# Performance work log

Hardware: AMD Instinct MI355X
Metric: run time of the kernel (lower is better)

Reference implementation:

```python
import jax, jax.numpy as jnp
import numpy as np

B, L, D, W = 4, 512, 768, 12
K = L * W  # number of candidate spans


def _mlp(x, w1, b1, w2, b2):
    # Linear -> ReLU -> (Dropout=identity in eval) -> Linear
    return jax.nn.relu(x @ w1.T + b1) @ w2.T + b2


def setup_inputs() -> dict:
    key = jax.random.key(0)
    ks = jax.random.split(key, 16)
    sc_d = 1.0 / np.sqrt(D)
    sc_4d = 1.0 / np.sqrt(4 * D)
    sc_2d = 1.0 / np.sqrt(2 * D)
    inp = {
        "h": jax.random.normal(ks[0], (B, L, D), dtype=jnp.float32),
        "span_idx": jax.random.randint(ks[1], (B, K, 2), 0, L, dtype=jnp.int64),
        # project_start: Linear(D,4D), Linear(4D,D)
        "ws1": jax.random.uniform(ks[2], (4 * D, D), jnp.float32, -sc_d, sc_d),
        "bs1": jax.random.uniform(ks[3], (4 * D,), jnp.float32, -sc_d, sc_d),
        "ws2": jax.random.uniform(ks[4], (D, 4 * D), jnp.float32, -sc_4d, sc_4d),
        "bs2": jax.random.uniform(ks[5], (D,), jnp.float32, -sc_4d, sc_4d),
        # project_end
        "we1": jax.random.uniform(ks[6], (4 * D, D), jnp.float32, -sc_d, sc_d),
        "be1": jax.random.uniform(ks[7], (4 * D,), jnp.float32, -sc_d, sc_d),
        "we2": jax.random.uniform(ks[8], (D, 4 * D), jnp.float32, -sc_4d, sc_4d),
        "be2": jax.random.uniform(ks[9], (D,), jnp.float32, -sc_4d, sc_4d),
        # out_project: Linear(2D,4D), Linear(4D,D)
        "wo1": jax.random.uniform(ks[10], (4 * D, 2 * D), jnp.float32, -sc_2d, sc_2d),
        "bo1": jax.random.uniform(ks[11], (4 * D,), jnp.float32, -sc_2d, sc_2d),
        "wo2": jax.random.uniform(ks[12], (D, 4 * D), jnp.float32, -sc_4d, sc_4d),
        "bo2": jax.random.uniform(ks[13], (D,), jnp.float32, -sc_4d, sc_4d),
    }
    return inp


def reference(h, span_idx, ws1, bs1, ws2, bs2, we1, be1, we2, be2, wo1, bo1, wo2, bo2):
    start_rep = _mlp(h, ws1, bs1, ws2, bs2)  # [B, L, D]
    end_rep = _mlp(h, we1, be1, we2, be2)    # [B, L, D]
    bidx = jnp.arange(B)[:, None]
    start_span = start_rep[bidx, span_idx[:, :, 0]]  # gather along seq dim -> [B, K, D]
    end_span = end_rep[bidx, span_idx[:, :, 1]]      # [B, K, D]
    cat = jax.nn.relu(jnp.concatenate([start_span, end_span], axis=-1))  # [B, K, 2D]
    out = _mlp(cat, wo1, bo1, wo2, bo2)  # [B, K, D]
    return out.reshape(B, L, W, D)
```

## Files before the change

### kernel.cpp

```cpp
#include <hip/hip_runtime.h>
#include <hip/hip_bf16.h>

using bf16 = __hip_bfloat16;
using bf16x8 = __attribute__((ext_vector_type(8))) __bf16;
using f32x4  = __attribute__((ext_vector_type(4))) float;
typedef unsigned short ushort_t;

#define BM 128
#define BN 128
#define BK 32


__device__ __forceinline__ void gl_lds16(const void* g, void* l) {
  __builtin_amdgcn_global_load_lds(
      (const __attribute__((address_space(1))) void*)g,
      (__attribute__((address_space(3))) void*)l, 16, 0, 0);
}

__device__ __forceinline__ ushort_t f2bf(float f) {
  unsigned u = __float_as_uint(f);
  u += 0x7FFF + ((u >> 16) & 1);
  return (ushort_t)(u >> 16);
}

__global__ void sniff(const unsigned* __restrict__ w1,
                      const unsigned* __restrict__ idx, int* flags) {
  __shared__ int cnt[2];
  if (threadIdx.x == 0) { cnt[0] = 0; cnt[1] = 0; }
  __syncthreads();
  int t = threadIdx.x;
  int c0 = 0;
  for (int k = 0; k < 4; ++k) {
    unsigned lo = w1[t * 4 + k] & 0xFFFFu;
    unsigned e = (lo >> 7) & 0xFF;
    if (e <= 122) c0++;
  }
  int c1 = (idx[2 * t + 1] != 0) ? 1 : 0;
  atomicAdd(&cnt[0], c0);
  atomicAdd(&cnt[1], c1);
  __syncthreads();
  if (threadIdx.x == 0) {
    flags[0] = (cnt[0] >= 900) ? 1 : 0;
    flags[1] = (cnt[1] == 0) ? 1 : 0;
  }
}

__global__ void norm_idx(const int* __restrict__ flags, const void* __restrict__ src,
                         int* __restrict__ dst) {
  int i = blockIdx.x * 256 + threadIdx.x;
  int v = flags[1] ? (int)((const long long*)src)[i] : ((const int*)src)[i];
  dst[i] = v;
}

__global__ void cvt_all(const int* __restrict__ flags,
                        const void* s0, const void* s1, const void* s2,
                        const void* s3, const void* s4, const void* s5,
                        const void* s6, ushort_t* __restrict__ dst) {
  long i = ((long)blockIdx.x * 256 + threadIdx.x) * 4;
  const void* src; long off;
  if      (i <  1572864) { src = s0; off = i; }
  else if (i <  3932160) { src = s1; off = i - 1572864; }
  else if (i <  6291456) { src = s2; off = i - 3932160; }
  else if (i <  8650752) { src = s3; off = i - 6291456; }
  else if (i < 11010048) { src = s4; off = i - 8650752; }
  else if (i < 15728640) { src = s5; off = i - 11010048; }
  else                   { src = s6; off = i - 15728640; }
  if (flags[0]) {
    *(ushort4*)(dst + i) = *((const ushort4*)((const ushort_t*)src + off));
  } else {
    float4 f = ((const float4*)src)[off >> 2];
    ushort4 o;
    o.x = f2bf(f.x); o.y = f2bf(f.y); o.z = f2bf(f.z); o.w = f2bf(f.w);
    *(ushort4*)(dst + i) = o;
  }
}

__global__ void cvt_bias(const int* __restrict__ flags,
                         const void* b0, const void* b1, const void* b2,
                         const void* b3, const void* b4, const void* b5,
                         float* __restrict__ dst) {
  int i = blockIdx.x * 256 + threadIdx.x;
  if (i >= 14592) return;
  if (i >= 11520) { dst[i] = 0.f; return; }
  const void* src; int off;
  if (i < 3072)       { src = b0; off = i; }
  else if (i < 3840)  { src = b1; off = i - 3072; }
  else if (i < 6912)  { src = b2; off = i - 3840; }
  else if (i < 7680)  { src = b3; off = i - 6912; }
  else if (i < 10752) { src = b4; off = i - 7680; }
  else                { src = b5; off = i - 10752; }
  dst[i] = flags[0] ? __bfloat162float(((const bf16*)src)[off])
                    : ((const float*)src)[off];
}

template <bool GATHER, bool RELU, bool OUTF32>
__global__ __launch_bounds__(256) void gemm_bt(
    const bf16* __restrict__ A, const bf16* __restrict__ A2,
    const bf16* __restrict__ repS, const bf16* __restrict__ repE,
    const int* __restrict__ sidx, int row_base,
    const bf16* __restrict__ Bw, const bf16* __restrict__ Bw2,
    const float* __restrict__ bias, const float* __restrict__ bias2,
    void* __restrict__ C, void* __restrict__ C2, int nsplit,
    int N, int Kdim, int bstride) {
  __shared__ bf16 lA[BM * BK];
  __shared__ bf16 lB[BN * BK];

  const int tid  = threadIdx.x;
  const int lane = tid & 63;
  const int wave = tid >> 6;
  const int wm = wave >> 1, wn = wave & 1;
  int by = blockIdx.y;
  const bf16* Bw_ = Bw; const float* bias_ = bias; void* C_ = C; const bf16* A_ = A;
  if (by >= nsplit) { by -= nsplit; Bw_ = Bw2; bias_ = bias2; C_ = C2; A_ = A2; }
  const int m0 = blockIdx.x * BM;
  const int n0 = by * BN;

  const int srow = tid >> 2;
  const int scol = 8 * ((tid & 3) ^ ((tid >> 3) & 3));

  const bf16 *a0 = nullptr, *a1 = nullptr;
  const bf16 *pS0 = nullptr, *pE0 = nullptr, *pS1 = nullptr, *pE1 = nullptr;
  if (GATHER) {
    int r0 = row_base + m0 + srow;
    int r1 = r0 + 64;
    int b0 = r0 / 6144, b1 = r1 / 6144;
    int s0 = min(max(sidx[2 * r0], 0), 511);
    int e0 = min(max(sidx[2 * r0 + 1], 0), 511);
    int s1 = min(max(sidx[2 * r1], 0), 511);
    int e1 = min(max(sidx[2 * r1 + 1], 0), 511);
    pS0 = repS + ((size_t)b0 * 512 + s0) * 768 + scol;
    pE0 = repE + ((size_t)b0 * 512 + e0) * 768 + scol;
    pS1 = repS + ((size_t)b1 * 512 + s1) * 768 + scol;
    pE1 = repE + ((size_t)b1 * 512 + e1) * 768 + scol;
  } else {
    a0 = A_ + (size_t)(m0 + srow) * Kdim + scol;
    a1 = a0 + (size_t)64 * Kdim;
  }
  const bf16* b0p = Bw_ + (size_t)(n0 + srow) * bstride + scol;
  const bf16* b1p = b0p + (size_t)64 * bstride;

  f32x4 acc[4][4];
  const f32x4 z = {0.f, 0.f, 0.f, 0.f};
#pragma unroll
  for (int i = 0; i < 4; ++i)
#pragma unroll
    for (int j = 0; j < 4; ++j) acc[i][j] = z;

  const int fr = lane & 15;
  const int fk = 8 * ((lane >> 4) ^ ((lane >> 1) & 3));

  for (int k0 = 0; k0 < Kdim; k0 += BK) {
    const bf16 *sa0, *sa1;
    if (GATHER) {
      if (k0 < 768) { sa0 = pS0 + k0; sa1 = pS1 + k0; }
      else          { sa0 = pE0 + (k0 - 768); sa1 = pE1 + (k0 - 768); }
    } else {
      sa0 = a0 + k0; sa1 = a1 + k0;
    }
    gl_lds16(sa0, lA + tid * 8);
    gl_lds16(sa1, lA + 2048 + tid * 8);
    gl_lds16(b0p + k0, lB + tid * 8);
    gl_lds16(b1p + k0, lB + 2048 + tid * 8);
    __syncthreads();

    bf16x8 af[4], bv[4];
#pragma unroll
    for (int i = 0; i < 4; ++i)
      af[i] = *(const bf16x8*)(const void*)(lA + (wm * 64 + i * 16 + fr) * BK + fk);
#pragma unroll
    for (int j = 0; j < 4; ++j)
      bv[j] = *(const bf16x8*)(const void*)(lB + (wn * 64 + j * 16 + fr) * BK + fk);
#pragma unroll
    for (int i = 0; i < 4; ++i)
#pragma unroll
      for (int j = 0; j < 4; ++j)
        acc[i][j] = __builtin_amdgcn_mfma_f32_16x16x32_bf16(af[i], bv[j], acc[i][j], 0, 0, 0);
    __syncthreads();
  }

  float* Cf = (float*)C_;
  bf16*  Cb = (bf16*)C_;
#pragma unroll
  for (int j = 0; j < 4; ++j) {
    int n = n0 + wn * 64 + j * 16 + fr;
    float bj = bias_[n];
#pragma unroll
    for (int i = 0; i < 4; ++i) {
      int mb = m0 + wm * 64 + i * 16 + (lane >> 4) * 4;
#pragma unroll
      for (int r = 0; r < 4; ++r) {
        float v = acc[i][j][r] + bj;
        if (RELU) v = fmaxf(v, 0.f);
        if (OUTF32) Cf[(size_t)(mb + r) * N + n] = v;
        else        Cb[(size_t)(mb + r) * N + n] = __float2bfloat16(v);
      }
    }
  }
}

__global__ __launch_bounds__(256) void gemm_final_fused(
    const ushort_t* __restrict__ Ps, const ushort_t* __restrict__ Pe,
    const int* __restrict__ sidx,
    const bf16* __restrict__ Bw, const float* __restrict__ bias,
    float* __restrict__ out) {
  __shared__ bf16 lA[2 * 4096];
  __shared__ bf16 lB[2 * 4096];

  const int tid  = threadIdx.x;
  const int lane = tid & 63;
  const int wave = tid >> 6;
  const int wm = wave >> 1, wn = wave & 1;
  const int m0 = blockIdx.x * BM;
  const int n0 = blockIdx.y * BN;

  const int srow = tid >> 2;
  const int scol = 8 * ((tid & 3) ^ ((tid >> 3) & 3));

  int r0 = m0 + srow, r1 = r0 + 64;
  int b0 = r0 / 6144, b1 = r1 / 6144;
  int s0 = min(max(sidx[2 * r0], 0), 511);
  int e0 = min(max(sidx[2 * r0 + 1], 0), 511);
  int s1 = min(max(sidx[2 * r1], 0), 511);
  int e1 = min(max(sidx[2 * r1 + 1], 0), 511);
  const ushort_t* pS0 = Ps + ((size_t)b0 * 512 + s0) * 3072 + scol;
  const ushort_t* pE0 = Pe + ((size_t)b0 * 512 + e0) * 3072 + scol;
  const ushort_t* pS1 = Ps + ((size_t)b1 * 512 + s1) * 3072 + scol;
  const ushort_t* pE1 = Pe + ((size_t)b1 * 512 + e1) * 3072 + scol;

  const bf16* bp0 = Bw + (size_t)(n0 + srow) * 3072 + scol;
  const bf16* bp1 = bp0 + (size_t)64 * 3072;

  f32x4 acc[4][4];
  const f32x4 z = {0.f, 0.f, 0.f, 0.f};
#pragma unroll
  for (int i = 0; i < 4; ++i)
#pragma unroll
    for (int j = 0; j < 4; ++j) acc[i][j] = z;

  const int fr = lane & 15;
  const int fk = 8 * ((lane >> 4) ^ ((lane >> 1) & 3));

  auto pack_store = [&](uint4 xs, uint4 xe, bf16* dst) {
    unsigned w[4];
    const unsigned* us = &xs.x;
    const unsigned* ue = &xe.x;
#pragma unroll
    for (int q = 0; q < 4; ++q) {
      float lo = __uint_as_float(us[q] << 16) + __uint_as_float(ue[q] << 16);
      float hi = __uint_as_float(us[q] & 0xFFFF0000u) +
                 __uint_as_float(ue[q] & 0xFFFF0000u);
      w[q] = (unsigned)f2bf(fmaxf(lo, 0.f)) |
             ((unsigned)f2bf(fmaxf(hi, 0.f)) << 16);
    }
    *(uint4*)(void*)dst = *(const uint4*)w;
  };

  {
    gl_lds16(bp0, lB + tid * 8);
    gl_lds16(bp1, lB + 2048 + tid * 8);
    uint4 xs0 = *(const uint4*)(const void*)pS0;
    uint4 xe0 = *(const uint4*)(const void*)pE0;
    uint4 xs1 = *(const uint4*)(const void*)pS1;
    uint4 xe1 = *(const uint4*)(const void*)pE1;
    pack_store(xs0, xe0, lA + tid * 8);
    pack_store(xs1, xe1, lA + 2048 + tid * 8);
    __syncthreads();
  }

  for (int it = 0; it < 96; ++it) {
    const int cur = (it & 1) << 12;
    const int nxt = ((it + 1) & 1) << 12;
    const int k1 = (it + 1) * BK;
    const bool pre = (it + 1) < 96;
    uint4 xs0, xe0, xs1, xe1;
    if (pre) {
      gl_lds16(bp0 + k1, lB + nxt + tid * 8);
      gl_lds16(bp1 + k1, lB + nxt + 2048 + tid * 8);
      xs0 = *(const uint4*)(const void*)(pS0 + k1);
      xe0 = *(const uint4*)(const void*)(pE0 + k1);
      xs1 = *(const uint4*)(const void*)(pS1 + k1);
      xe1 = *(const uint4*)(const void*)(pE1 + k1);
    }

    bf16x8 af[4], bv[4];
#pragma unroll
    for (int i = 0; i < 4; ++i)
      af[i] = *(const bf16x8*)(const void*)(lA + cur + (wm * 64 + i * 16 + fr) * BK + fk);
#pragma unroll
    for (int j = 0; j < 4; ++j)
      bv[j] = *(const bf16x8*)(const void*)(lB + cur + (wn * 64 + j * 16 + fr) * BK + fk);
#pragma unroll
    for (int i = 0; i < 4; ++i)
#pragma unroll
      for (int j = 0; j < 4; ++j)
        acc[i][j] = __builtin_amdgcn_mfma_f32_16x16x32_bf16(af[i], bv[j], acc[i][j], 0, 0, 0);

    if (pre) {
      pack_store(xs0, xe0, lA + nxt + tid * 8);
      pack_store(xs1, xe1, lA + nxt + 2048 + tid * 8);
    }
    __syncthreads();
  }

#pragma unroll
  for (int j = 0; j < 4; ++j) {
    int n = n0 + wn * 64 + j * 16 + fr;
    float bj = bias[n];
#pragma unroll
    for (int i = 0; i < 4; ++i) {
      int mb = m0 + wm * 64 + i * 16 + (lane >> 4) * 4;
#pragma unroll
      for (int r = 0; r < 4; ++r)
        out[(size_t)(mb + r) * 768 + n] = acc[i][j][r] + bj;
    }
  }
}

extern "C" void kernel_launch(void* const* d_in, const int* in_sizes, int n_in,
                              void* d_out, int out_size, void* d_ws, size_t ws_size,
                              hipStream_t stream) {
  const void* h    = d_in[0];
  const void* sidx = d_in[1];
  const void *ws1 = d_in[2],  *bs1 = d_in[3];
  const void *ws2 = d_in[4],  *bs2 = d_in[5];
  const void *we1 = d_in[6],  *be1 = d_in[7];
  const void *we2 = d_in[8],  *be2 = d_in[9];
  const void *wo1 = d_in[10], *bo1 = d_in[11];
  const void *wo2 = d_in[12], *bo2 = d_in[13];

  char* p = (char*)d_ws;
  int*      flags = (int*)p;
  int*      idx32 = (int*)(p + 256);
  float*    biasf = (float*)(p + 256 + 196608);
  ushort_t* hb    = (ushort_t*)(p + 256 + 196608 + 65536);
  ushort_t* w1sb  = hb   + (size_t)1572864;
  ushort_t* w2sb  = w1sb + (size_t)2359296;
  ushort_t* w1eb  = w2sb + (size_t)2359296;
  ushort_t* w2eb  = w1eb + (size_t)2359296;
  ushort_t* wo1b  = w2eb + (size_t)2359296;
  ushort_t* wo2b  = wo1b + (size_t)4718592;
  ushort_t* repS  = wo2b + (size_t)2359296;
  ushort_t* repE  = repS + (size_t)1572864;
  char*     R     = (char*)(repE + (size_t)1572864);
  size_t fixed = (size_t)(R - (char*)d_ws);
  if (ws_size < fixed) return;
  size_t Rsz = ws_size - fixed;

  const size_t P_BF = (size_t)2 * 2048 * 3072 * 2;
  int tier = (Rsz >= P_BF) ? 2 : 3;

  dim3 blk(256);
  const int XBIG = 0x40000000;
  sniff<<<1, blk, 0, stream>>>((const unsigned*)ws1, (const unsigned*)sidx, flags);
  norm_idx<<<192, blk, 0, stream>>>(flags, sidx, idx32);
  cvt_all<<<17664, blk, 0, stream>>>(flags, h, ws1, ws2, we1, we2, wo1, wo2, hb);
  cvt_bias<<<57, blk, 0, stream>>>(flags, bs1, bs2, be1, be2, bo1, bo2, biasf);
  const float *bs1f = biasf, *bs2f = biasf + 3072, *be1f = biasf + 3840,
              *be2f = biasf + 6912, *bo1f = biasf + 7680, *bo2f = biasf + 10752,
              *zerof = biasf + 11520;
  float* outf = (float*)d_out;

  if (tier == 2) {
    ushort_t* hidS = (ushort_t*)R;
    ushort_t* hidE = hidS + (size_t)2048 * 3072;
    gemm_bt<false, true, false><<<dim3(16, 48), blk, 0, stream>>>(
        (const bf16*)hb, (const bf16*)hb, nullptr, nullptr, nullptr, 0,
        (const bf16*)w1sb, (const bf16*)w1eb, bs1f, be1f,
        hidS, hidE, 24, 3072, 768, 768);
    gemm_bt<false, true, false><<<dim3(16, 12), blk, 0, stream>>>(
        (const bf16*)hidS, (const bf16*)hidE, nullptr, nullptr, nullptr, 0,
        (const bf16*)w2sb, (const bf16*)w2eb, bs2f, be2f,
        (bf16*)repS, (bf16*)repE, 6, 768, 3072, 3072);
    ushort_t* Ps = (ushort_t*)R;
    ushort_t* Pe = Ps + (size_t)2048 * 3072;
    gemm_bt<false, false, false><<<dim3(16, 48), blk, 0, stream>>>(
        (const bf16*)repS, (const bf16*)repE, nullptr, nullptr, nullptr, 0,
        (const bf16*)wo1b, (const bf16*)wo1b + 768, bo1f, zerof,
        Ps, Pe, 24, 3072, 768, 1536);
    gemm_final_fused<<<dim3(192, 6), blk, 0, stream>>>(
        Ps, Pe, idx32, (const bf16*)wo2b, bo2f, outf);
  } else {
    long long cT = (long long)(Rsz / ((size_t)2 * 3072 * 2));
    cT = (cT / 128) * 128; if (cT > 2048) cT = 2048;
    long long cO = (long long)(Rsz / ((size_t)3072 * 2));
    cO = (cO / 128) * 128; if (cO > 24576) cO = 24576;
    if (cT < 128 || cO < 128) return;
    ushort_t* scr = (ushort_t*)R;
    for (long long r = 0; r < 2048; r += cT) {
      long long mc = 2048 - r < cT ? 2048 - r : cT;
      ushort_t* hidS = scr;
      ushort_t* hidE = scr + (size_t)cT * 3072;
      gemm_bt<false, true, false><<<dim3(mc / 128, 48), blk, 0, stream>>>(
          (const bf16*)hb + r * 768, (const bf16*)hb + r * 768,
          nullptr, nullptr, nullptr, 0,
          (const bf16*)w1sb, (const bf16*)w1eb, bs1f, be1f,
          hidS, hidE, 24, 3072, 768, 768);
      gemm_bt<false, true, false><<<dim3(mc / 128, 12), blk, 0, stream>>>(
          (const bf16*)hidS, (const bf16*)hidE, nullptr, nullptr, nullptr, 0,
          (const bf16*)w2sb, (const bf16*)w2eb, bs2f, be2f,
          (bf16*)repS + r * 768, (bf16*)repE + r * 768, 6, 768, 3072, 3072);
    }
    for (long long r = 0; r < 24576; r += cO) {
      long long mc = 24576 - r < cO ? 24576 - r : cO;
      gemm_bt<true, true, false><<<dim3(mc / 128, 24), blk, 0, stream>>>(
          nullptr, nullptr, (const bf16*)repS, (const bf16*)repE, idx32, (int)r,
          (const bf16*)wo1b, nullptr, bo1f, nullptr,
          scr, nullptr, XBIG, 3072, 1536, 1536);
      gemm_bt<false, false, true><<<dim3(mc / 128, 6), blk, 0, stream>>>(
          (const bf16*)scr, nullptr, nullptr, nullptr, nullptr, 0,
          (const bf16*)wo2b, nullptr, bo2f, nullptr,
          outf + (size_t)r * 768, nullptr, XBIG, 768, 3072, 3072);
    }
  }
}
```

Measured before the change: 557.7 us.

## Widen final fused GEMM tile to 256 columns to halve gather work

The final gather+GEMM kernel now computes a 128x256 output tile per block instead of 128x128. Each gathered and summed activation row is reused across twice as many output columns, so the span gather, add, ReLU and convert work is done half as often. The grid drops to 3 column blocks, accumulator registers double, and LDS for B doubles. The bf16 packing also switches to a single hardware pack-convert instruction, and launch bounds request 2 blocks per SIMD. The larger register footprint may reduce occupancy or cause spills.

```diff
diff --git a/kernel.cpp b/kernel.cpp
--- a/kernel.cpp
+++ b/kernel.cpp
@@ -198,20 +198,20 @@
   }
 }
 
-__global__ __launch_bounds__(256) void gemm_final_fused(
+__global__ __launch_bounds__(256, 2) void gemm_final_fused(
     const ushort_t* __restrict__ Ps, const ushort_t* __restrict__ Pe,
     const int* __restrict__ sidx,
     const bf16* __restrict__ Bw, const float* __restrict__ bias,
     float* __restrict__ out) {
   __shared__ bf16 lA[2 * 4096];
-  __shared__ bf16 lB[2 * 4096];
+  __shared__ bf16 lB[2 * 8192];
 
   const int tid  = threadIdx.x;
   const int lane = tid & 63;
   const int wave = tid >> 6;
   const int wm = wave >> 1, wn = wave & 1;
   const int m0 = blockIdx.x * BM;
-  const int n0 = blockIdx.y * BN;
+  const int n0 = blockIdx.y * 256;
 
   const int srow = tid >> 2;
   const int scol = 8 * ((tid & 3) ^ ((tid >> 3) & 3));
@@ -229,13 +229,15 @@
 
   const bf16* bp0 = Bw + (size_t)(n0 + srow) * 3072 + scol;
   const bf16* bp1 = bp0 + (size_t)64 * 3072;
-
-  f32x4 acc[4][4];
+  const bf16* bp2 = bp0 + (size_t)128 * 3072;
+  const bf16* bp3 = bp0 + (size_t)192 * 3072;
+
+  f32x4 acc[4][8];
   const f32x4 z = {0.f, 0.f, 0.f, 0.f};
 #pragma unroll
   for (int i = 0; i < 4; ++i)
 #pragma unroll
-    for (int j = 0; j < 4; ++j) acc[i][j] = z;
+    for (int j = 0; j < 8; ++j) acc[i][j] = z;
 
   const int fr = lane & 15;
   const int fk = 8 * ((lane >> 4) ^ ((lane >> 1) & 3));
@@ -246,11 +248,10 @@
     const unsigned* ue = &xe.x;
 #pragma unroll
     for (int q = 0; q < 4; ++q) {
-      float lo = __uint_as_float(us[q] << 16) + __uint_as_float(ue[q] << 16);
-      float hi = __uint_as_float(us[q] & 0xFFFF0000u) +
-                 __uint_as_float(ue[q] & 0xFFFF0000u);
-      w[q] = (unsigned)f2bf(fmaxf(lo, 0.f)) |
-             ((unsigned)f2bf(fmaxf(hi, 0.f)) << 16);
+      float lo = fmaxf(__uint_as_float(us[q] << 16) + __uint_as_float(ue[q] << 16), 0.f);
+      float hi = fmaxf(__uint_as_float(us[q] & 0xFFFF0000u) +
+                       __uint_as_float(ue[q] & 0xFFFF0000u), 0.f);
+      asm("v_cvt_pk_bf16_f32 %0, %1, %2" : "=v"(w[q]) : "v"(lo), "v"(hi));
     }
     *(uint4*)(void*)dst = *(const uint4*)w;
   };
@@ -258,6 +259,8 @@
   {
     gl_lds16(bp0, lB + tid * 8);
     gl_lds16(bp1, lB + 2048 + tid * 8);
+    gl_lds16(bp2, lB + 4096 + tid * 8);
+    gl_lds16(bp3, lB + 6144 + tid * 8);
     uint4 xs0 = *(const uint4*)(const void*)pS0;
     uint4 xe0 = *(const uint4*)(const void*)pE0;
     uint4 xs1 = *(const uint4*)(const void*)pS1;
@@ -268,43 +271,46 @@
   }
 
   for (int it = 0; it < 96; ++it) {
-    const int cur = (it & 1) << 12;
-    const int nxt = ((it + 1) & 1) << 12;
+    const int curA = (it & 1) << 12;
+    const int curB = (it & 1) << 13;
+    const int nxtA = ((it + 1) & 1) << 12;
+    const int nxtB = ((it + 1) & 1) << 13;
     const int k1 = (it + 1) * BK;
     const bool pre = (it + 1) < 96;
     uint4 xs0, xe0, xs1, xe1;
     if (pre) {
-      gl_lds16(bp0 + k1, lB + nxt + tid * 8);
-      gl_lds16(bp1 + k1, lB + nxt + 2048 + tid * 8);
+      gl_lds16(bp0 + k1, lB + nxtB + tid * 8);
+      gl_lds16(bp1 + k1, lB + nxtB + 2048 + tid * 8);
+      gl_lds16(bp2 + k1, lB + nxtB + 4096 + tid * 8);
+      gl_lds16(bp3 + k1, lB + nxtB + 6144 + tid * 8);
       xs0 = *(const uint4*)(const void*)(pS0 + k1);
       xe0 = *(const uint4*)(const void*)(pE0 + k1);
       xs1 = *(const uint4*)(const void*)(pS1 + k1);
       xe1 = *(const uint4*)(const void*)(pE1 + k1);
     }
 
-    bf16x8 af[4], bv[4];
+    bf16x8 af[4];
 #pragma unroll
     for (int i = 0; i < 4; ++i)
-      af[i] = *(const bf16x8*)(const void*)(lA + cur + (wm * 64 + i * 16 + fr) * BK + fk);
-#pragma unroll
-    for (int j = 0; j < 4; ++j)
-      bv[j] = *(const bf16x8*)(const void*)(lB + cur + (wn * 64 + j * 16 + fr) * BK + fk);
-#pragma unroll
-    for (int i = 0; i < 4; ++i)
-#pragma unroll
-      for (int j = 0; j < 4; ++j)
-        acc[i][j] = __builtin_amdgcn_mfma_f32_16x16x32_bf16(af[i], bv[j], acc[i][j], 0, 0, 0);
+      af[i] = *(const bf16x8*)(const void*)(lA + curA + (wm * 64 + i * 16 + fr) * BK + fk);
+#pragma unroll
+    for (int j = 0; j < 8; ++j) {
+      bf16x8 bv = *(const bf16x8*)(const void*)(lB + curB + (wn * 128 + j * 16 + fr) * BK + fk);
+#pragma unroll
+      for (int i = 0; i < 4; ++i)
+        acc[i][j] = __builtin_amdgcn_mfma_f32_16x16x32_bf16(af[i], bv, acc[i][j], 0, 0, 0);
+    }
 
     if (pre) {
-      pack_store(xs0, xe0, lA + nxt + tid * 8);
-      pack_store(xs1, xe1, lA + nxt + 2048 + tid * 8);
+      pack_store(xs0, xe0, lA + nxtA + tid * 8);
+      pack_store(xs1, xe1, lA + nxtA + 2048 + tid * 8);
     }
     __syncthreads();
   }
 
 #pragma unroll
-  for (int j = 0; j < 4; ++j) {
-    int n = n0 + wn * 64 + j * 16 + fr;
+  for (int j = 0; j < 8; ++j) {
+    int n = n0 + wn * 128 + j * 16 + fr;
     float bj = bias[n];
 #pragma unroll
     for (int i = 0; i < 4; ++i) {
@@ -377,7 +383,7 @@
         (const bf16*)repS, (const bf16*)repE, nullptr, nullptr, nullptr, 0,
         (const bf16*)wo1b, (const bf16*)wo1b + 768, bo1f, zerof,
         Ps, Pe, 24, 3072, 768, 1536);
-    gemm_final_fused<<<dim3(192, 6), blk, 0, stream>>>(
+    gemm_final_fused<<<dim3(192, 3), blk, 0, stream>>>(
         Ps, Pe, idx32, (const bf16*)wo2b, bo2f, outf);
   } else {
     long long cT = (long long)(Rsz / ((size_t)2 * 3072 * 2));
```

After: 553.7 us. No clear change (-0.7%).
